# Performance work log

Measured on AMD Instinct MI355X. Metric: run time of the kernel, lower is better.

The kernel has to match this reference:

```python
import jax, jax.numpy as jnp
import numpy as np

DIM = 1024
N_HEADS = 16
HEAD_DIM = DIM // N_HEADS
LORA_DIM = 16
B, T = 4, 1024


def _rope(x):
    # x: [B, H, T, D] with D even; rotate first/second halves (torch impl style)
    D = x.shape[-1]
    half = D // 2
    theta = 1.0 / (10000.0 ** (jnp.arange(0, D, 2, dtype=jnp.float32) / D))  # [D/2]
    pos = jnp.arange(x.shape[-2], dtype=jnp.float32)                         # [T]
    pt = pos[:, None] * theta[None, :]                                       # [T, D/2]
    sin, cos = jnp.sin(pt), jnp.cos(pt)
    xr, xi = x[..., :half], x[..., half:]
    return jnp.concatenate([xr * cos - xi * sin, xr * sin + xi * cos], axis=-1)


def setup_inputs() -> dict:
    key = jax.random.key(0)
    ks = jax.random.split(key, 16)
    def n(k, shape, std=0.02):
        return jax.random.normal(k, shape, jnp.float32) * std
    return {
        "x": jax.random.normal(ks[0], (B, T, DIM), jnp.float32),
        "q_w": n(ks[1], (DIM, DIM)),
        "k_w": n(ks[2], (DIM, DIM)),
        "v_w": n(ks[3], (DIM, DIM)),
        "q_a": n(ks[4], (LORA_DIM, DIM), 0.001),
        "q_b": n(ks[5], (DIM, LORA_DIM), 0.001),
        "q_l": jax.random.normal(ks[6], (DIM,), jnp.float32),
        "k_a": n(ks[7], (LORA_DIM, DIM), 0.001),
        "k_b": n(ks[8], (DIM, LORA_DIM), 0.001),
        "k_l": jax.random.normal(ks[9], (DIM,), jnp.float32),
        "v_a": n(ks[10], (LORA_DIM, DIM), 0.001),
        "v_b": n(ks[11], (DIM, LORA_DIM), 0.001),
        "v_l": jax.random.normal(ks[12], (DIM,), jnp.float32),
        "proj_w": n(ks[13], (DIM, DIM)),
        "proj_b": n(ks[14], (DIM,)),
    }


def reference(x, q_w, k_w, v_w, q_a, q_b, q_l, k_a, k_b, k_l,
              v_a, v_b, v_l, proj_w, proj_b):
    Bb, Tt, C = x.shape
    # token shift: xx[t] = x[t-1], xx[0] = 0 (ZeroPad2d((0,0,1,-1)))
    xx = jnp.pad(x, ((0, 0), (1, 0), (0, 0)))[:, :Tt]
    xxx = xx - x

    def lora(a, b, lam):
        return lam + jnp.tanh(x @ a.T) @ b.T  # [B,T,C]

    q = (x + xxx * lora(q_a, q_b, q_l)) @ q_w.T
    k = (x + xxx * lora(k_a, k_b, k_l)) @ k_w.T
    v = (x + xxx * lora(v_a, v_b, v_l)) @ v_w.T

    def split_heads(t):
        return t.reshape(Bb, Tt, N_HEADS, HEAD_DIM).transpose(0, 2, 1, 3)  # [B,H,T,D]

    q = _rope(split_heads(q))
    k = _rope(split_heads(k))
    v = split_heads(v)

    scale = 1.0 / np.sqrt(HEAD_DIM).astype(np.float32)
    scores = jnp.einsum('bhqd,bhkd->bhqk', q, k) * scale
    causal = jnp.tril(jnp.ones((Tt, Tt), dtype=bool))
    scores = jnp.where(causal, scores, jnp.float32(-1e30))
    att = jax.nn.softmax(scores, axis=-1)
    out = jnp.einsum('bhqk,bhkd->bhqd', att, v)
    out = out.transpose(0, 2, 1, 3).reshape(Bb, Tt, C)
    return out @ proj_w.T + proj_b
```

## Files before the change

### kernel.cpp

```cpp
#include <hip/hip_runtime.h>
#include <hip/hip_bf16.h>

typedef __hip_bfloat16 bf16;
typedef __attribute__((ext_vector_type(8))) short bf16x8;
typedef __attribute__((ext_vector_type(4))) float f32x4;

typedef const __attribute__((address_space(1))) unsigned int* gp_t;
typedef __attribute__((address_space(3))) unsigned int* lp_t;

__device__ __forceinline__ bf16 tobf(float f) { return __float2bfloat16(f); }
__device__ __forceinline__ float tof(bf16 h) { return __bfloat162float(h); }

__device__ __forceinline__ short bfbits(float f) {
    bf16 h = __float2bfloat16(f);
    return *reinterpret_cast<short*>(&h);
}
__device__ __forceinline__ bf16x8 pack8(float4 a, float4 b) {
    bf16x8 r;
    r[0] = bfbits(a.x); r[1] = bfbits(a.y); r[2] = bfbits(a.z); r[3] = bfbits(a.w);
    r[4] = bfbits(b.x); r[5] = bfbits(b.y); r[6] = bfbits(b.z); r[7] = bfbits(b.w);
    return r;
}

__device__ __forceinline__ void gload_lds16(const void* g, void* l) {
    __builtin_amdgcn_global_load_lds((gp_t)g, (lp_t)l, 16, 0, 0);
}

__global__ __launch_bounds__(256) void lora_gate_fused(
    const float* x,
    const float* qa, const float* ka, const float* va,
    const float* qbw, const float* ql,
    const float* kbw, const float* kl,
    const float* vbw, const float* vl,
    const float* qw, const float* kw, const float* vw, const float* pw,
    bf16* wdst,
    bf16* xqo, bf16* xko, bf16* xvo) {
    const int XS = 1028;
    int row0 = blockIdx.x * 8;
    int t0 = row0 & 1023;
    int tid = threadIdx.x;
    int wave = tid >> 6, lane = tid & 63;
    int quad = lane >> 4, l16 = lane & 15;

    __shared__ float sx[9 * 1028];
    __shared__ float spT[3][4][8][17];
    __shared__ float sT[8 * 48];

    {
        int prow = (row0 == 0) ? 0 : row0 - 1;
        for (int i = 0; i < 9; ++i) {
            int grow = (i == 0) ? prow : row0 + i - 1;
            gload_lds16(x + (size_t)grow * 1024 + wave * 256 + lane * 4,
                        &sx[i * XS + wave * 256]);
        }
    }
    {
        int m = blockIdx.x >> 7;
        const float* src = m == 0 ? qw : (m == 1 ? kw : (m == 2 ? vw : pw));
        bf16* dst = wdst + (size_t)m * (1u << 20);
        int off = (blockIdx.x & 127) * 8192;
#pragma unroll
        for (int u = 0; u < 8; ++u) {
            int i = off + u * 1024 + tid * 4;
            float4 f = *(const float4*)(src + i);
            ushort4 o4;
            o4.x = (unsigned short)bfbits(f.x);
            o4.y = (unsigned short)bfbits(f.y);
            o4.z = (unsigned short)bfbits(f.z);
            o4.w = (unsigned short)bfbits(f.w);
            *(ushort4*)&dst[i] = o4;
        }
    }
    __syncthreads();

    {
        int xr = (l16 < 8) ? l16 : 7;
        f32x4 acc[3];
#pragma unroll
        for (int m = 0; m < 3; m++) acc[m] = (f32x4){0.f, 0.f, 0.f, 0.f};
        int kb = wave * 256;
#pragma unroll
        for (int kk = 0; kk < 256; kk += 32) {
            int k0 = kb + kk;
            const float* xs = &sx[(1 + xr) * XS + k0 + quad * 8];
            bf16x8 af = pack8(*(const float4*)xs, *(const float4*)(xs + 4));
#pragma unroll
            for (int m = 0; m < 3; m++) {
                const float* am = m == 0 ? qa : (m == 1 ? ka : va);
                const float* as = am + (size_t)l16 * 1024 + k0 + quad * 8;
                bf16x8 bf_ = pack8(*(const float4*)as, *(const float4*)(as + 4));
                acc[m] = __builtin_amdgcn_mfma_f32_16x16x32_bf16(af, bf_, acc[m], 0, 0, 0);
            }
        }
#pragma unroll
        for (int m = 0; m < 3; m++)
#pragma unroll
            for (int r = 0; r < 4; r++) {
                int row = quad * 4 + r;
                if (row < 8) spT[m][wave][row][l16] = acc[m][r];
            }
    }
    __syncthreads();
    if (tid < 384) {
        int m = tid >> 7, idx = tid & 127;
        int row = idx >> 4, col = idx & 15;
        float v = spT[m][0][row][col] + spT[m][1][row][col]
                + spT[m][2][row][col] + spT[m][3][row][col];
        sT[row * 48 + m * 16 + col] = tanhf(v);
    }
    __syncthreads();

#pragma unroll
    for (int u = 0; u < 4; ++u) {
        int d = tid + u * 256;
        float qbv[16], kbv[16], vbv[16];
#pragma unroll
        for (int p = 0; p < 4; ++p) {
            *(float4*)&qbv[p * 4] = *(const float4*)(qbw + (size_t)d * 16 + p * 4);
            *(float4*)&kbv[p * 4] = *(const float4*)(kbw + (size_t)d * 16 + p * 4);
            *(float4*)&vbv[p * 4] = *(const float4*)(vbw + (size_t)d * 16 + p * 4);
        }
        float qlv = ql[d], klv = kl[d], vlv = vl[d];
        float xp = (t0 == 0) ? 0.f : sx[0 * XS + d];
        for (int rr = 0; rr < 8; ++rr) {
            float xc = sx[(rr + 1) * XS + d];
            float dx = xp - xc;
            float gq = qlv, gk = klv, gv = vlv;
#pragma unroll
            for (int j = 0; j < 16; ++j) {
                gq += sT[rr * 48 + j] * qbv[j];
                gk += sT[rr * 48 + 16 + j] * kbv[j];
                gv += sT[rr * 48 + 32 + j] * vbv[j];
            }
            size_t o = (size_t)(row0 + rr) * 1024 + d;
            xqo[o] = tobf(xc + dx * gq);
            xko[o] = tobf(xc + dx * gk);
            xvo[o] = tobf(xc + dx * gv);
            xp = xc;
        }
    }
}

__global__ __launch_bounds__(256) void gemm128(
    const bf16* A0, const bf16* A1, const bf16* A2,
    const bf16* W0, const bf16* W1, const bf16* W2,
    bf16* C0, bf16* C1, bf16* C2,
    const float* bias, float* outF, int proj, int zcnt) {
    const int K = 1024;
    int ppx = (zcnt * 32) >> 3;
    int xcd = blockIdx.x & 7;
    int j = blockIdx.x >> 3;
    int pair = xcd * ppx + (j >> 3);
    int n0 = (j & 7) * 128;
    int bz = pair >> 5;
    int m0 = (pair & 31) * 128;

    const bf16* A = bz == 0 ? A0 : (bz == 1 ? A1 : A2);
    const bf16* W = bz == 0 ? W0 : (bz == 1 ? W1 : W2);
    bf16* C = bz == 0 ? C0 : (bz == 1 ? C1 : C2);

    __shared__ alignas(16) bf16 sA[64 * 64];
    __shared__ alignas(16) bf16 sB[64 * 64];

    int wave = threadIdx.x >> 6, lane = threadIdx.x & 63;
    int quad = lane >> 4, l16 = lane & 15;

    f32x4 acc[4][4];
#pragma unroll
    for (int i = 0; i < 4; i++)
#pragma unroll
        for (int j2 = 0; j2 < 4; j2++) acc[i][j2] = (f32x4){0.f, 0.f, 0.f, 0.f};

    int Rb0 = wave * 16 + (lane >> 3);
    int s0 = lane & 7;

    auto stage = [&](int k0) {
#pragma unroll
        for (int p = 0; p < 2; p++) {
            int R = Rb0 + p * 8;
            int cs = s0 ^ (R & 7);
            int mr = 2 * R + (cs >> 2);
            int kc = (cs & 3) * 8;
            gload_lds16(A + (size_t)(m0 + mr) * K + k0 + kc, &sA[(wave * 16 + p * 8) * 64]);
            gload_lds16(W + (size_t)(n0 + mr) * K + k0 + kc, &sB[(wave * 16 + p * 8) * 64]);
        }
    };

    int mw = (wave >> 1) * 64, nw = (wave & 1) * 64;
    int slot = (((l16 & 1) << 2) | quad) ^ ((l16 >> 1) & 7);
    int abase = ((mw >> 1) + (l16 >> 1)) * 64 + slot * 8;
    int bbase = ((nw >> 1) + (l16 >> 1)) * 64 + slot * 8;

    for (int it = 0; it < 32; ++it) {
        __syncthreads();
        stage(it * 32);
        __syncthreads();
        bf16x8 af[4], bfr[4];
#pragma unroll
        for (int f = 0; f < 4; f++) {
            af[f] = *(const bf16x8*)&sA[abase + f * 512];
            bfr[f] = *(const bf16x8*)&sB[bbase + f * 512];
        }
#pragma unroll
        for (int i = 0; i < 4; i++)
#pragma unroll
            for (int j2 = 0; j2 < 4; j2++)
                acc[i][j2] = __builtin_amdgcn_mfma_f32_16x16x32_bf16(af[i], bfr[j2], acc[i][j2], 0, 0, 0);
    }

    if (proj) {
#pragma unroll
        for (int i = 0; i < 4; i++) {
            int mrow = m0 + mw + i * 16 + quad * 4;
#pragma unroll
            for (int j2 = 0; j2 < 4; j2++) {
                int col = n0 + nw + j2 * 16 + l16;
                float bv = bias[col];
#pragma unroll
                for (int r = 0; r < 4; r++)
                    outF[(size_t)(mrow + r) * 1024 + col] = acc[i][j2][r] + bv;
            }
        }
    } else if (bz < 2) {
        float sc = (bz == 0) ? 0.125f : 1.0f;
        int tb = ((m0 + mw) & 1023) + quad * 4;
#pragma unroll
        for (int j2 = 0; j2 < 2; j2++) {
            int d = j2 * 16 + l16;
            float theta = __expf(-(float)d * (9.210340371976184f / 32.0f));
            float s1, c1, s16, c16, st, ct;
            sincosf(theta, &s1, &c1);
            sincosf(16.0f * theta, &s16, &c16);
            sincosf((float)tb * theta, &st, &ct);
            int col = n0 + nw + j2 * 16 + l16;
#pragma unroll
            for (int i = 0; i < 4; i++) {
                int mrow = m0 + mw + i * 16 + quad * 4;
                float c = ct, s = st;
#pragma unroll
                for (int r = 0; r < 4; r++) {
                    float xr = acc[i][j2][r], xi = acc[i][j2 + 2][r];
                    C[(size_t)(mrow + r) * 1024 + col] = tobf((xr * c - xi * s) * sc);
                    C[(size_t)(mrow + r) * 1024 + col + 32] = tobf((xr * s + xi * c) * sc);
                    float cn = c * c1 - s * s1;
                    s = s * c1 + c * s1;
                    c = cn;
                }
                float cn = ct * c16 - st * s16;
                st = st * c16 + ct * s16;
                ct = cn;
            }
        }
    } else {
#pragma unroll
        for (int i = 0; i < 4; i++) {
            int mrow = m0 + mw + i * 16 + quad * 4;
#pragma unroll
            for (int j2 = 0; j2 < 4; j2++) {
                int col = n0 + nw + j2 * 16 + l16;
                ushort4 o4;
                o4.x = (unsigned short)bfbits(acc[i][j2][0]);
                o4.y = (unsigned short)bfbits(acc[i][j2][1]);
                o4.z = (unsigned short)bfbits(acc[i][j2][2]);
                o4.w = (unsigned short)bfbits(acc[i][j2][3]);
                *(ushort4*)&C[(size_t)col * 4096 + mrow] = o4;
            }
        }
    }
}

__global__ __launch_bounds__(256) void attention(const bf16* Qm, const bf16* Km,
                                                 const bf16* Vt, bf16* attn) {
    int gid = blockIdx.x;
    int qblk = 15 - (gid >> 6);
    int bh = (((gid >> 3) & 7) << 3) | (gid & 7);
    int b = bh >> 4, h = bh & 15;
    int wave = threadIdx.x >> 6, lane = threadIdx.x & 63;
    int quad = lane >> 4, l16 = lane & 15;
    int m7 = l16 & 7;

    const bf16* Qb = Qm + (size_t)b * 1024 * 1024 + h * 64;
    const bf16* Kb = Km + (size_t)b * 1024 * 1024 + h * 64;
    const bf16* Vb = Vt + (size_t)(h * 64) * 4096 + b * 1024;

    __shared__ alignas(16) bf16 sK[2][64 * 64];
    __shared__ alignas(16) bf16 sV[2][64 * 64];
    __shared__ alignas(16) bf16 sP[4][16 * 64];

    int srow = lane >> 3;
    int scol = ((lane & 7) ^ srow) * 8;

    auto stage = [&](int kt, int bufi) {
#pragma unroll
        for (int p = 0; p < 2; p++) {
            int rbase = p * 32 + wave * 8;
            gload_lds16(Kb + (size_t)(kt * 64 + rbase + srow) * 1024 + scol, &sK[bufi][rbase * 64]);
            gload_lds16(Vb + (size_t)(rbase + srow) * 4096 + kt * 64 + scol, &sV[bufi][rbase * 64]);
        }
    };

    int qrow0 = qblk * 64 + wave * 16;
    bf16x8 aq0 = *(const bf16x8*)&Qb[(size_t)(qrow0 + l16) * 1024 + quad * 8];
    bf16x8 aq1 = *(const bf16x8*)&Qb[(size_t)(qrow0 + l16) * 1024 + quad * 8 + 32];

    f32x4 o[4];
#pragma unroll
    for (int nt = 0; nt < 4; nt++) o[nt] = (f32x4){0.f, 0.f, 0.f, 0.f};
    float lpart[4] = {0.f, 0.f, 0.f, 0.f};

    stage(0, 0);

    int buf = 0;
    for (int kt = 0; kt <= qblk; ++kt, buf ^= 1) {
        __syncthreads();
        if (kt < qblk) stage(kt + 1, buf ^ 1);

        f32x4 S[4];
#pragma unroll
        for (int j = 0; j < 4; j++) {
            int row = j * 16 + l16;
            bf16x8 bk0 = *(const bf16x8*)&sK[buf][row * 64 + ((quad ^ m7) * 8)];
            bf16x8 bk1 = *(const bf16x8*)&sK[buf][row * 64 + (((quad + 4) ^ m7) * 8)];
            f32x4 z = __builtin_amdgcn_mfma_f32_16x16x32_bf16(aq0, bk0, (f32x4){0.f, 0.f, 0.f, 0.f}, 0, 0, 0);
            S[j] = __builtin_amdgcn_mfma_f32_16x16x32_bf16(aq1, bk1, z, 0, 0, 0);
        }
        if (kt == qblk) {
#pragma unroll
            for (int j = 0; j < 4; j++) {
                int key = kt * 64 + j * 16 + l16;
#pragma unroll
                for (int r = 0; r < 4; r++) {
                    int qr = qrow0 + quad * 4 + r;
                    if (key > qr) S[j][r] = -3.0e38f;
                }
            }
        }
#pragma unroll
        for (int j = 0; j < 4; j++)
#pragma unroll
            for (int r = 0; r < 4; r++) {
                float p = __expf(S[j][r]);
                S[j][r] = p;
                lpart[r] += p;
            }

#pragma unroll
        for (int j = 0; j < 4; j++) {
            int c = j * 2 + (l16 >> 3);
#pragma unroll
            for (int r = 0; r < 4; r++) {
                int prow = quad * 4 + r;
                sP[wave][prow * 64 + ((c ^ (prow & 7)) * 8) + m7] = tobf(S[j][r]);
            }
        }
        asm volatile("s_waitcnt lgkmcnt(0)" ::: "memory");
        bf16x8 ap0 = *(const bf16x8*)&sP[wave][l16 * 64 + ((quad ^ m7) * 8)];
        bf16x8 ap1 = *(const bf16x8*)&sP[wave][l16 * 64 + (((quad + 4) ^ m7) * 8)];
#pragma unroll
        for (int nt = 0; nt < 4; nt++) {
            int row = nt * 16 + l16;
            bf16x8 bv0 = *(const bf16x8*)&sV[buf][row * 64 + ((quad ^ m7) * 8)];
            bf16x8 bv1 = *(const bf16x8*)&sV[buf][row * 64 + (((quad + 4) ^ m7) * 8)];
            o[nt] = __builtin_amdgcn_mfma_f32_16x16x32_bf16(ap0, bv0, o[nt], 0, 0, 0);
            o[nt] = __builtin_amdgcn_mfma_f32_16x16x32_bf16(ap1, bv1, o[nt], 0, 0, 0);
        }
    }

    float invl[4];
#pragma unroll
    for (int r = 0; r < 4; r++) {
        float v = lpart[r];
        v += __shfl_xor(v, 1);
        v += __shfl_xor(v, 2);
        v += __shfl_xor(v, 4);
        v += __shfl_xor(v, 8);
        invl[r] = 1.0f / v;
    }
#pragma unroll
    for (int nt = 0; nt < 4; nt++)
#pragma unroll
        for (int r = 0; r < 4; r++) {
            int t = qrow0 + quad * 4 + r;
            int col = h * 64 + nt * 16 + l16;
            attn[(size_t)(b * 1024 + t) * 1024 + col] = tobf(o[nt][r] * invl[r]);
        }
}

extern "C" void kernel_launch(void* const* d_in, const int* in_sizes, int n_in,
                              void* d_out, int out_size, void* d_ws, size_t ws_size,
                              hipStream_t stream) {
    const float* x = (const float*)d_in[0];
    const float* qw = (const float*)d_in[1];
    const float* kw = (const float*)d_in[2];
    const float* vw = (const float*)d_in[3];
    const float* qa = (const float*)d_in[4];
    const float* qb = (const float*)d_in[5];
    const float* ql = (const float*)d_in[6];
    const float* ka = (const float*)d_in[7];
    const float* kb = (const float*)d_in[8];
    const float* kl = (const float*)d_in[9];
    const float* va = (const float*)d_in[10];
    const float* vb = (const float*)d_in[11];
    const float* vl = (const float*)d_in[12];
    const float* pw = (const float*)d_in[13];
    const float* pb = (const float*)d_in[14];
    float* out = (float*)d_out;

    char* ws = (char*)d_ws;
    const size_t MB = 1024 * 1024;
    bf16* wqb = (bf16*)ws;
    bf16* wkb = wqb + 1048576;
    bf16* wvb = wkb + 1048576;
    bf16* wpb = wvb + 1048576;
    bf16* xqb = (bf16*)(ws + 8 * MB);
    bf16* xkb = xqb + 4194304;
    bf16* xvb = xkb + 4194304;
    bf16* qm = (bf16*)(ws + 32 * MB);
    bf16* km = qm + 4194304;
    bf16* Vt = km + 4194304;
    bf16* attn = xqb;

    lora_gate_fused<<<512, 256, 0, stream>>>(x, qa, ka, va, qb, ql, kb, kl, vb, vl,
                                             qw, kw, vw, pw, wqb,
                                             xqb, xkb, xvb);
    gemm128<<<768, 256, 0, stream>>>(xqb, xkb, xvb, wqb, wkb, wvb, qm, km, Vt,
                                     nullptr, nullptr, 0, 3);
    attention<<<1024, 256, 0, stream>>>(qm, km, Vt, attn);
    gemm128<<<256, 256, 0, stream>>>(attn, nullptr, nullptr, wpb, nullptr, nullptr,
                                     nullptr, nullptr, nullptr, pb, out, 1, 1);
}
```

Before: 204.6 us.

## Split LoRA gate kernel into tanh-projection and gating kernels

The fused LoRA/gate kernel is split in two. The first kernel computes tanh(x·A^T) for 64 rows per block, using all 16 MFMA rows instead of only 8, and writes the result to a global scratch buffer; extra blocks in the same launch convert the weights to bf16. A second kernel reads that buffer and applies the gated token-shift mix over 32 rows by 256 columns per block, holding x in registers. This removes the wasted half of the MFMA tile and the large shared-memory footprint that limited occupancy, at the cost of an extra launch, a global round trip for the small T buffer, and re-reading x from global memory.

```diff
diff --git a/kernel.cpp b/kernel.cpp
--- a/kernel.cpp
+++ b/kernel.cpp
@@ -26,39 +26,19 @@
     __builtin_amdgcn_global_load_lds((gp_t)g, (lp_t)l, 16, 0, 0);
 }
 
-__global__ __launch_bounds__(256) void lora_gate_fused(
+__global__ __launch_bounds__(256) void lora_t_wconv(
     const float* x,
     const float* qa, const float* ka, const float* va,
-    const float* qbw, const float* ql,
-    const float* kbw, const float* kl,
-    const float* vbw, const float* vl,
     const float* qw, const float* kw, const float* vw, const float* pw,
-    bf16* wdst,
-    bf16* xqo, bf16* xko, bf16* xvo) {
-    const int XS = 1028;
-    int row0 = blockIdx.x * 8;
-    int t0 = row0 & 1023;
+    bf16* wdst, float* Tg) {
     int tid = threadIdx.x;
-    int wave = tid >> 6, lane = tid & 63;
-    int quad = lane >> 4, l16 = lane & 15;
-
-    __shared__ float sx[9 * 1028];
-    __shared__ float spT[3][4][8][17];
-    __shared__ float sT[8 * 48];
-
-    {
-        int prow = (row0 == 0) ? 0 : row0 - 1;
-        for (int i = 0; i < 9; ++i) {
-            int grow = (i == 0) ? prow : row0 + i - 1;
-            gload_lds16(x + (size_t)grow * 1024 + wave * 256 + lane * 4,
-                        &sx[i * XS + wave * 256]);
-        }
-    }
-    {
-        int m = blockIdx.x >> 7;
+
+    if (blockIdx.x >= 64) {
+        int cblk = blockIdx.x - 64;
+        int m = cblk >> 7;
         const float* src = m == 0 ? qw : (m == 1 ? kw : (m == 2 ? vw : pw));
         bf16* dst = wdst + (size_t)m * (1u << 20);
-        int off = (blockIdx.x & 127) * 8192;
+        int off = (cblk & 127) * 8192;
 #pragma unroll
         for (int u = 0; u < 8; ++u) {
             int i = off + u * 1024 + tid * 4;
@@ -70,74 +50,95 @@
             o4.w = (unsigned short)bfbits(f.w);
             *(ushort4*)&dst[i] = o4;
         }
-    }
+        return;
+    }
+
+    int wave = tid >> 6, lane = tid & 63;
+    int quad = lane >> 4, l16 = lane & 15;
+    int row0 = blockIdx.x * 64;
+
+    const float* xb = x + (size_t)(row0 + wave * 16 + l16) * 1024 + quad * 8;
+    const float* qab = qa + (size_t)l16 * 1024 + quad * 8;
+    const float* kab = ka + (size_t)l16 * 1024 + quad * 8;
+    const float* vab = va + (size_t)l16 * 1024 + quad * 8;
+
+    f32x4 acc[3];
+#pragma unroll
+    for (int m = 0; m < 3; m++) acc[m] = (f32x4){0.f, 0.f, 0.f, 0.f};
+
+#pragma unroll 4
+    for (int kk = 0; kk < 1024; kk += 32) {
+        bf16x8 af = pack8(*(const float4*)(xb + kk), *(const float4*)(xb + kk + 4));
+        bf16x8 bq = pack8(*(const float4*)(qab + kk), *(const float4*)(qab + kk + 4));
+        bf16x8 bk = pack8(*(const float4*)(kab + kk), *(const float4*)(kab + kk + 4));
+        bf16x8 bv = pack8(*(const float4*)(vab + kk), *(const float4*)(vab + kk + 4));
+        acc[0] = __builtin_amdgcn_mfma_f32_16x16x32_bf16(af, bq, acc[0], 0, 0, 0);
+        acc[1] = __builtin_amdgcn_mfma_f32_16x16x32_bf16(af, bk, acc[1], 0, 0, 0);
+        acc[2] = __builtin_amdgcn_mfma_f32_16x16x32_bf16(af, bv, acc[2], 0, 0, 0);
+    }
+
+#pragma unroll
+    for (int m = 0; m < 3; m++)
+#pragma unroll
+        for (int r = 0; r < 4; r++) {
+            int row = row0 + wave * 16 + quad * 4 + r;
+            Tg[(size_t)row * 48 + m * 16 + l16] = tanhf(acc[m][r]);
+        }
+}
+
+__global__ __launch_bounds__(256) void lora_gate(
+    const float* x, const float* Tg,
+    const float* qbw, const float* ql,
+    const float* kbw, const float* kl,
+    const float* vbw, const float* vl,
+    bf16* xqo, bf16* xko, bf16* xvo) {
+    int tb = blockIdx.x >> 2, dc = blockIdx.x & 3;
+    int row0 = tb * 32, d0 = dc * 256;
+    int tid = threadIdx.x;
+    int d = d0 + tid;
+
+    __shared__ float sTT[32 * 48];
+
+    for (int i = tid; i < 384; i += 256)
+        *(float4*)&sTT[i * 4] = *(const float4*)&Tg[(size_t)row0 * 48 + i * 4];
+
+    float qbv[16], kbv[16], vbv[16];
+#pragma unroll
+    for (int p = 0; p < 4; ++p) {
+        *(float4*)&qbv[p * 4] = *(const float4*)(qbw + (size_t)d * 16 + p * 4);
+        *(float4*)&kbv[p * 4] = *(const float4*)(kbw + (size_t)d * 16 + p * 4);
+        *(float4*)&vbv[p * 4] = *(const float4*)(vbw + (size_t)d * 16 + p * 4);
+    }
+    float qlv = ql[d], klv = kl[d], vlv = vl[d];
+
+    float xv[32];
+#pragma unroll
+    for (int i = 0; i < 32; ++i) xv[i] = x[(size_t)(row0 + i) * 1024 + d];
+    int prow = (row0 == 0) ? 0 : row0 - 1;
+    float xpv = x[(size_t)prow * 1024 + d];
+    float xp = ((row0 & 1023) == 0) ? 0.f : xpv;
+
     __syncthreads();
 
-    {
-        int xr = (l16 < 8) ? l16 : 7;
-        f32x4 acc[3];
-#pragma unroll
-        for (int m = 0; m < 3; m++) acc[m] = (f32x4){0.f, 0.f, 0.f, 0.f};
-        int kb = wave * 256;
-#pragma unroll
-        for (int kk = 0; kk < 256; kk += 32) {
-            int k0 = kb + kk;
-            const float* xs = &sx[(1 + xr) * XS + k0 + quad * 8];
-            bf16x8 af = pack8(*(const float4*)xs, *(const float4*)(xs + 4));
-#pragma unroll
-            for (int m = 0; m < 3; m++) {
-                const float* am = m == 0 ? qa : (m == 1 ? ka : va);
-                const float* as = am + (size_t)l16 * 1024 + k0 + quad * 8;
-                bf16x8 bf_ = pack8(*(const float4*)as, *(const float4*)(as + 4));
-                acc[m] = __builtin_amdgcn_mfma_f32_16x16x32_bf16(af, bf_, acc[m], 0, 0, 0);
-            }
-        }
-#pragma unroll
-        for (int m = 0; m < 3; m++)
-#pragma unroll
-            for (int r = 0; r < 4; r++) {
-                int row = quad * 4 + r;
-                if (row < 8) spT[m][wave][row][l16] = acc[m][r];
-            }
-    }
-    __syncthreads();
-    if (tid < 384) {
-        int m = tid >> 7, idx = tid & 127;
-        int row = idx >> 4, col = idx & 15;
-        float v = spT[m][0][row][col] + spT[m][1][row][col]
-                + spT[m][2][row][col] + spT[m][3][row][col];
-        sT[row * 48 + m * 16 + col] = tanhf(v);
-    }
-    __syncthreads();
-
-#pragma unroll
-    for (int u = 0; u < 4; ++u) {
-        int d = tid + u * 256;
-        float qbv[16], kbv[16], vbv[16];
+#pragma unroll
+    for (int rr = 0; rr < 32; ++rr) {
+        float xc = xv[rr];
+        float dx = xp - xc;
+        float gq = qlv, gk = klv, gv = vlv;
 #pragma unroll
         for (int p = 0; p < 4; ++p) {
-            *(float4*)&qbv[p * 4] = *(const float4*)(qbw + (size_t)d * 16 + p * 4);
-            *(float4*)&kbv[p * 4] = *(const float4*)(kbw + (size_t)d * 16 + p * 4);
-            *(float4*)&vbv[p * 4] = *(const float4*)(vbw + (size_t)d * 16 + p * 4);
-        }
-        float qlv = ql[d], klv = kl[d], vlv = vl[d];
-        float xp = (t0 == 0) ? 0.f : sx[0 * XS + d];
-        for (int rr = 0; rr < 8; ++rr) {
-            float xc = sx[(rr + 1) * XS + d];
-            float dx = xp - xc;
-            float gq = qlv, gk = klv, gv = vlv;
-#pragma unroll
-            for (int j = 0; j < 16; ++j) {
-                gq += sT[rr * 48 + j] * qbv[j];
-                gk += sT[rr * 48 + 16 + j] * kbv[j];
-                gv += sT[rr * 48 + 32 + j] * vbv[j];
-            }
-            size_t o = (size_t)(row0 + rr) * 1024 + d;
-            xqo[o] = tobf(xc + dx * gq);
-            xko[o] = tobf(xc + dx * gk);
-            xvo[o] = tobf(xc + dx * gv);
-            xp = xc;
-        }
+            float4 tq = *(const float4*)&sTT[rr * 48 + p * 4];
+            float4 tk = *(const float4*)&sTT[rr * 48 + 16 + p * 4];
+            float4 tv = *(const float4*)&sTT[rr * 48 + 32 + p * 4];
+            gq += tq.x * qbv[p * 4] + tq.y * qbv[p * 4 + 1] + tq.z * qbv[p * 4 + 2] + tq.w * qbv[p * 4 + 3];
+            gk += tk.x * kbv[p * 4] + tk.y * kbv[p * 4 + 1] + tk.z * kbv[p * 4 + 2] + tk.w * kbv[p * 4 + 3];
+            gv += tv.x * vbv[p * 4] + tv.y * vbv[p * 4 + 1] + tv.z * vbv[p * 4 + 2] + tv.w * vbv[p * 4 + 3];
+        }
+        size_t o = (size_t)(row0 + rr) * 1024 + d;
+        xqo[o] = tobf(xc + dx * gq);
+        xko[o] = tobf(xc + dx * gk);
+        xvo[o] = tobf(xc + dx * gv);
+        xp = xc;
     }
 }
 
@@ -419,10 +420,10 @@
     bf16* km = qm + 4194304;
     bf16* Vt = km + 4194304;
     bf16* attn = xqb;
-
-    lora_gate_fused<<<512, 256, 0, stream>>>(x, qa, ka, va, qb, ql, kb, kl, vb, vl,
-                                             qw, kw, vw, pw, wqb,
-                                             xqb, xkb, xvb);
+    float* Tg = (float*)(ws + 32 * MB);
+
+    lora_t_wconv<<<576, 256, 0, stream>>>(x, qa, ka, va, qw, kw, vw, pw, wqb, Tg);
+    lora_gate<<<512, 256, 0, stream>>>(x, Tg, qb, ql, kb, kl, vb, vl, xqb, xkb, xvb);
     gemm128<<<768, 256, 0, stream>>>(xqb, xkb, xvb, wqb, wkb, wvb, qm, km, Vt,
                                      nullptr, nullptr, 0, 3);
     attention<<<1024, 256, 0, stream>>>(qm, km, Vt, attn);
```

Result: slower. 236.6 us (+15.6%).
